# Performance work log

Measured on AMD Instinct MI355X. Metric: run time of the kernel, lower is better.

The kernel has to match this reference:

```python
import jax, jax.numpy as jnp
import numpy as np

NUM_HEADS = 4

def setup_inputs() -> dict:
    key = jax.random.key(0)
    ks = jax.random.split(key, 5)
    B, T, F, C = 2, 128, 256, 256
    # weights scaled ~1/sqrt(C) so softmax is not saturated
    s = 1.0 / np.sqrt(C)
    return {
        "x": jax.random.normal(ks[0], (B, T, F, C), jnp.float32),
        "w_in": jax.random.normal(ks[1], (3 * C, C), jnp.float32) * s,
        "b_in": jax.random.normal(ks[2], (3 * C,), jnp.float32) * 0.01,
        "w_out": jax.random.normal(ks[3], (C, C), jnp.float32) * s,
        "b_out": jax.random.normal(ks[4], (C,), jnp.float32) * 0.01,
        "band": 16,
    }

def reference(x, w_in, b_in, w_out, b_out, band):
    B, T, F, C = x.shape
    H = NUM_HEADS
    D = C // H
    x2 = x.reshape(B * T, F, C)  # attention over frequency, independent per (B,T)
    qkv = x2 @ w_in.T + b_in  # [BT, F, 3C]
    q, k, v = jnp.split(qkv, 3, axis=-1)
    def heads(t):
        return t.reshape(B * T, F, H, D).transpose(0, 2, 1, 3)  # [BT, H, F, D]
    q, k, v = heads(q), heads(k), heads(v)
    scores = jnp.einsum('bhid,bhjd->bhij', q, k) / jnp.sqrt(jnp.asarray(D, x.dtype))
    i = jnp.arange(F)[:, None]
    j = jnp.arange(F)[None, :]
    keep = jnp.abs(i - j) <= band  # banded locality mask [F, F]
    scores = jnp.where(keep, scores, -jnp.inf)
    attn = jax.nn.softmax(scores, axis=-1)
    out = jnp.einsum('bhij,bhjd->bhid', attn, v)  # [BT, H, F, D]
    out = out.transpose(0, 2, 1, 3).reshape(B * T, F, C)
    y = out @ w_out.T + b_out
    return y.reshape(B, T, F, C)
```

## Files before the change

### kernel.cpp

```cpp
#include <hip/hip_runtime.h>
#include <hip/hip_bf16.h>
#include <cstdint>

typedef unsigned int u32;
typedef __attribute__((ext_vector_type(8))) __bf16 bf16x8;
typedef __attribute__((ext_vector_type(4))) float f32x4;
typedef __attribute__((ext_vector_type(2))) _Float16 half2_t;
typedef __attribute__((ext_vector_type(4))) _Float16 half4;
typedef __attribute__((ext_vector_type(2))) __fp16 fp16x2;

#define BT_N 256
#define F_N 256
#define C_N 256
#define H_N 4
#define D_N 64
#define TC_N 768
#define M_N (BT_N * F_N)
#define VT_ST 268

__device__ __forceinline__ ushort f2bf(float f) {
  u32 u = __float_as_uint(f);
  u32 r = (u + 0x7fffu + ((u >> 16) & 1u)) >> 16;
  return (ushort)r;
}

__device__ __forceinline__ u32 pkbf(float a, float b) {
  return (u32)f2bf(a) | ((u32)f2bf(b) << 16);
}

__device__ __forceinline__ void gload_lds16(const ushort* g, ushort* l) {
  __builtin_amdgcn_global_load_lds(
      (const __attribute__((address_space(1))) u32*)g,
      (__attribute__((address_space(3))) u32*)l, 16, 0, 0);
}

#define WAITV(N) asm volatile("s_waitcnt vmcnt(" #N ")" ::: "memory")
#define BAR_IN  { __builtin_amdgcn_s_barrier(); \
                  asm volatile("" ::: "memory"); \
                  __builtin_amdgcn_sched_barrier(0); }
#define BAR_OUT { __builtin_amdgcn_sched_barrier(0); \
                  asm volatile("" ::: "memory"); \
                  __builtin_amdgcn_s_barrier(); }

__global__ __launch_bounds__(256) void cvt3_f32_bf16_k(
    const float* __restrict__ sx, ushort* __restrict__ dx, int nx4,
    const float* __restrict__ si, ushort* __restrict__ di, int ni4,
    const float* __restrict__ so, ushort* __restrict__ dq, int no4) {
  int idx = blockIdx.x * 256 + threadIdx.x;
  int stride = gridDim.x * 256;
  int ntot = nx4 + ni4 + no4;
  for (int i = idx; i < ntot; i += stride) {
    const float4* s;
    ushort* d;
    if (i < nx4) { s = (const float4*)sx + i; d = dx + (size_t)i * 4; }
    else if (i < nx4 + ni4) { int k = i - nx4; s = (const float4*)si + k; d = di + (size_t)k * 4; }
    else { int k = i - nx4 - ni4; s = (const float4*)so + k; d = dq + (size_t)k * 4; }
    float4 v = *s;
    *(uint2*)d = make_uint2(pkbf(v.x, v.y), pkbf(v.z, v.w));
  }
}

__global__ __launch_bounds__(256, 4) void gemm_qkv_sb(
    const ushort* __restrict__ Ap, const ushort* __restrict__ Bp,
    const float* __restrict__ bias, _Float16* __restrict__ Cp,
    int NTN, int nwg8) {
  __shared__ ushort smemH[128 * 64 * 2];

  const int tid = threadIdx.x;
  const int lane = tid & 63;
  const int wid = tid >> 6;
  const int wr = wid >> 1, wc = wid & 1;
  const int l15 = lane & 15, l4 = lane >> 4;
  const int b = blockIdx.x;
  const int bid = (b & 7) * nwg8 + (b >> 3);
  const int tm = bid / NTN;
  const int tn = bid - tm * NTN;
  const int rowBase = tm * 128, colBase = tn * 128;

  f32x4 acc[4][4] = {};

  const int ar = (tid >> 3);
  const int c8 = tid & 7;
  const int akk = ((c8 ^ (ar & 7)) << 3);
  const ushort* gB = Bp + (size_t)(colBase + ar) * 256 + akk;
  const ushort* gAh = Ap + (size_t)(rowBase + ar) * 256 + akk;

#pragma unroll
  for (int t = 0; t < 4; ++t) {
    const int k0 = t * 64;
#pragma unroll
    for (int c = 0; c < 4; ++c) {
      gload_lds16(gAh + (size_t)(c * 32) * 256 + k0,
                  smemH + (size_t)(c * 256 + (wid << 6)) * 8);
      gload_lds16(gB + (size_t)(c * 32) * 256 + k0,
                  smemH + 8192 + (size_t)(c * 256 + (wid << 6)) * 8);
    }
    __syncthreads();
    const ushort* As_ = smemH;
    const ushort* Bs_ = smemH + 8192;
#pragma unroll
    for (int kk = 0; kk < 2; ++kk) {
      bf16x8 af[4];
      bf16x8 bfr[4];
#pragma unroll
      for (int i2 = 0; i2 < 4; ++i2) {
        int row = wr * 64 + i2 * 16 + l15;
        af[i2] = *(const bf16x8*)(As_ + row * 64 + (((kk * 4 + l4) ^ (l15 & 7)) * 8));
      }
#pragma unroll
      for (int j2 = 0; j2 < 4; ++j2) {
        int row = wc * 64 + j2 * 16 + l15;
        bfr[j2] = *(const bf16x8*)(Bs_ + row * 64 + (((kk * 4 + l4) ^ (l15 & 7)) * 8));
      }
#pragma unroll
      for (int i2 = 0; i2 < 4; ++i2)
#pragma unroll
        for (int j2 = 0; j2 < 4; ++j2)
          acc[i2][j2] = __builtin_amdgcn_mfma_f32_16x16x32_bf16(
              af[i2], bfr[j2], acc[i2][j2], 0, 0, 0);
    }
    __syncthreads();
  }

  ushort* eb = smemH;
#pragma unroll
  for (int pass = 0; pass < 2; ++pass) {
#pragma unroll
    for (int jh = 0; jh < 2; ++jh) {
      const int i2 = pass * 2 + jh;
#pragma unroll
      for (int j2 = 0; j2 < 4; ++j2) {
        float bv = bias[colBase + wc * 64 + j2 * 16 + l15];
#pragma unroll
        for (int r = 0; r < 4; ++r) {
          _Float16 h = (_Float16)(acc[i2][j2][r] + bv);
          eb[(wr * 32 + jh * 16 + l4 * 4 + r) * 136 + wc * 64 + j2 * 16 + l15] =
              __builtin_bit_cast(ushort, h);
        }
      }
    }
    __syncthreads();
#pragma unroll
    for (int i = 0; i < 8; ++i) {
      int br = wid * 16 + 2 * i + (lane >> 5);
      int hl = lane & 31;
      uint2 d = *(const uint2*)(eb + br * 136 + hl * 4);
      int grow = rowBase + (br >> 5) * 64 + pass * 32 + (br & 31);
      *(uint2*)(Cp + (size_t)grow * TC_N + colBase + hl * 4) = d;
    }
    __syncthreads();
  }
}

template <typename OutT>
__global__ __launch_bounds__(256, 2) void gemm_bt(
    const ushort* __restrict__ Ap, const ushort* __restrict__ Bp,
    const float* __restrict__ bias, OutT* __restrict__ Cp,
    int N, int NTN, int nwg8) {
  constexpr bool F32OUT = (sizeof(OutT) == 4);
  constexpr int SMEM_BYTES = F32OUT ? 67584 : 65536;
  __shared__ char smem[SMEM_BYTES];
  ushort* smemH = (ushort*)smem;

  const int tid = threadIdx.x;
  const int lane = tid & 63;
  const int wid = tid >> 6;
  const int wr = wid >> 1, wc = wid & 1;
  const int l15 = lane & 15, l4 = lane >> 4;
  const int b = blockIdx.x;
  const int bid = (b & 7) * nwg8 + (b >> 3);
  const int tm = bid / NTN;
  const int tn = bid - tm * NTN;
  const int rowBase = tm * 128, colBase = tn * 128;

  f32x4 acc[4][4] = {};

  const int ar = (tid >> 3);
  const int c8 = tid & 7;
  const int akk = ((c8 ^ (ar & 7)) << 3);
  const ushort* gB = Bp + (size_t)(colBase + ar) * 256 + akk;
  const ushort* gAh = Ap + (size_t)(rowBase + ar) * 256 + akk;

#define STAGE_AB(buf, k0)                                                     \
  {                                                                           \
    ushort* As_ = smemH + (buf) * 8192;                                       \
    ushort* Bs_ = smemH + 16384 + (buf) * 8192;                               \
    _Pragma("unroll") for (int c = 0; c < 4; ++c) {                           \
      gload_lds16(gAh + (size_t)(c * 32) * 256 + (k0),                        \
                  As_ + (size_t)(c * 256 + (wid << 6)) * 8);                  \
      gload_lds16(gB + (size_t)(c * 32) * 256 + (k0),                         \
                  Bs_ + (size_t)(c * 256 + (wid << 6)) * 8);                  \
    }                                                                         \
  }

  STAGE_AB(0, 0);

  int cur = 0;
#pragma unroll
  for (int t = 0; t < 4; ++t) {
    if (t < 3) {
      STAGE_AB(cur ^ 1, (t + 1) * 64);
      WAITV(8);
    } else {
      WAITV(0);
    }
    BAR_IN;
    const ushort* As_ = smemH + cur * 8192;
    const ushort* Bs_ = smemH + 16384 + cur * 8192;
#pragma unroll
    for (int kk = 0; kk < 2; ++kk) {
      bf16x8 af[4];
      bf16x8 bfr[4];
#pragma unroll
      for (int i2 = 0; i2 < 4; ++i2) {
        int row = wr * 64 + i2 * 16 + l15;
        af[i2] = *(const bf16x8*)(As_ + row * 64 + (((kk * 4 + l4) ^ (l15 & 7)) * 8));
      }
#pragma unroll
      for (int j2 = 0; j2 < 4; ++j2) {
        int row = wc * 64 + j2 * 16 + l15;
        bfr[j2] = *(const bf16x8*)(Bs_ + row * 64 + (((kk * 4 + l4) ^ (l15 & 7)) * 8));
      }
#pragma unroll
      for (int i2 = 0; i2 < 4; ++i2)
#pragma unroll
        for (int j2 = 0; j2 < 4; ++j2)
          acc[i2][j2] = __builtin_amdgcn_mfma_f32_16x16x32_bf16(
              af[i2], bfr[j2], acc[i2][j2], 0, 0, 0);
    }
    BAR_OUT;
    cur ^= 1;
  }
#undef STAGE_AB

  __syncthreads();
  if constexpr (F32OUT) {
    float* eb = (float*)smem;
#pragma unroll
    for (int j2 = 0; j2 < 4; ++j2) {
      float bv = bias[colBase + wc * 64 + j2 * 16 + l15];
#pragma unroll
      for (int i2 = 0; i2 < 4; ++i2)
#pragma unroll
        for (int r = 0; r < 4; ++r)
          eb[(wr * 64 + i2 * 16 + l4 * 4 + r) * 132 + wc * 64 + j2 * 16 + l15] =
              acc[i2][j2][r] + bv;
    }
    __syncthreads();
#pragma unroll
    for (int i = 0; i < 32; ++i) {
      int row = wid * 32 + i;
      uint2 d = *(const uint2*)((const u32*)eb + row * 132 + lane * 2);
      *(uint2*)((float*)Cp + (size_t)(rowBase + row) * N + colBase + lane * 2) = d;
    }
  } else {
    ushort* eb = smemH;
#pragma unroll
    for (int j2 = 0; j2 < 4; ++j2) {
      float bv = bias[colBase + wc * 64 + j2 * 16 + l15];
#pragma unroll
      for (int i2 = 0; i2 < 4; ++i2)
#pragma unroll
        for (int r = 0; r < 4; ++r) {
          _Float16 h = (_Float16)(acc[i2][j2][r] + bv);
          eb[(wr * 64 + i2 * 16 + l4 * 4 + r) * 136 + wc * 64 + j2 * 16 + l15] =
              __builtin_bit_cast(ushort, h);
        }
    }
    __syncthreads();
#pragma unroll
    for (int i = 0; i < 16; ++i) {
      int row = wid * 32 + 2 * i + (lane >> 5);
      int hl = lane & 31;
      uint2 d = *(const uint2*)(eb + row * 136 + hl * 4);
      *(uint2*)((_Float16*)Cp + (size_t)(rowBase + row) * N + colBase + hl * 4) = d;
    }
  }
}

__global__ __launch_bounds__(256) void attn_mfma(
    const _Float16* __restrict__ qkv, ushort* __restrict__ aout) {
  __shared__ ushort smem[18432 + 64 * VT_ST];
  const int tid = threadIdx.x;
  const int bt = blockIdx.x >> 2;
  const int h = blockIdx.x & 3;
  const _Float16* base = qkv + (size_t)bt * 256 * 768 + h * 64;
  ushort* klds = smem;
  ushort* vlds = smem + 18432;

  {
    const int r0 = tid >> 3, c8 = tid & 7;
#pragma unroll
    for (int p = 0; p < 8; ++p) {
      int j = p * 32 + r0;
      const uint4 k4 = *(const uint4*)(base + (size_t)j * 768 + 256 + c8 * 8);
      *(uint4*)(klds + j * 72 + c8 * 8) = k4;
      const uint4 v4 = *(const uint4*)(base + (size_t)j * 768 + 512 + c8 * 8);
      const ushort* vh = (const ushort*)&v4;
      ushort* vtp = vlds + (c8 * 8) * VT_ST + j;
#pragma unroll
      for (int i = 0; i < 8; ++i) vtp[i * VT_ST] = vh[i];
    }
  }

  const int w = tid >> 6, lane = tid & 63;
  const int l15 = lane & 15, g = lane >> 4, g4 = g * 4;

  uint2 qf0[4], qf1[4], qf2[4], qf3[4];
  {
    const uint2* q0 = (const uint2*)(base + (size_t)(w * 64 + 0 * 16 + l15) * 768 + g4);
    const uint2* q1 = (const uint2*)(base + (size_t)(w * 64 + 1 * 16 + l15) * 768 + g4);
    const uint2* q2 = (const uint2*)(base + (size_t)(w * 64 + 2 * 16 + l15) * 768 + g4);
    const uint2* q3 = (const uint2*)(base + (size_t)(w * 64 + 3 * 16 + l15) * 768 + g4);
#pragma unroll
    for (int ks = 0; ks < 4; ++ks) {
      qf0[ks] = q0[ks * 4]; qf1[ks] = q1[ks * 4];
      qf2[ks] = q2[ks * 4]; qf3[ks] = q3[ks * 4];
    }
  }

  u32 bb = 0;
#pragma unroll
  for (int jt = 0; jt < 3; ++jt)
#pragma unroll
    for (int r = 0; r < 4; ++r) {
      int d = 16 * jt + g4 + r - 16 - l15;
      if (d >= -16 && d <= 16) bb |= 1u << (jt * 4 + r);
    }

  __syncthreads();

  const float SC = 0.18033688f;

#pragma unroll
  for (int rt = 0; rt < 4; ++rt) {
    const int R0 = w * 64 + rt * 16;
    const int Jc = R0 - 16;
    const uint2* qf = (rt == 0) ? qf0 : (rt == 1) ? qf1 : (rt == 2) ? qf2 : qf3;

    f32x4 st[3] = {};
#pragma unroll
    for (int jt = 0; jt < 3; ++jt) {
      int krow = Jc + 16 * jt + l15;
      krow = krow < 0 ? 0 : (krow > 255 ? 255 : krow);
      const ushort* kp = klds + krow * 72 + g4;
#pragma unroll
      for (int ks = 0; ks < 4; ++ks) {
        uint2 kf = *(const uint2*)(kp + ks * 16);
        st[jt] = __builtin_amdgcn_mfma_f32_16x16x16f16(
            __builtin_bit_cast(half4, kf), __builtin_bit_cast(half4, qf[ks]),
            st[jt], 0, 0, 0);
      }
    }

    float l_acc = 0.f;
    float pp[3][4];
#pragma unroll
    for (int jt = 0; jt < 3; ++jt)
#pragma unroll
      for (int r = 0; r < 4; ++r) {
        int jg = Jc + 16 * jt + g4 + r;
        bool keep = (((bb >> (jt * 4 + r)) & 1u) != 0) && (jg >= 0) && (jg < 256);
        float pv = keep ? __builtin_amdgcn_exp2f(st[jt][r] * SC) : 0.f;
        pp[jt][r] = pv;
        l_acc += pv;
      }
    l_acc += __shfl_xor(l_acc, 16, 64);
    l_acc += __shfl_xor(l_acc, 32, 64);
    const float inv = 1.f / l_acc;

    uint2 pf[3];
#pragma unroll
    for (int jt = 0; jt < 3; ++jt) {
      fp16x2 a = __builtin_amdgcn_cvt_pkrtz(pp[jt][0] * inv, pp[jt][1] * inv);
      fp16x2 c = __builtin_amdgcn_cvt_pkrtz(pp[jt][2] * inv, pp[jt][3] * inv);
      pf[jt].x = __builtin_bit_cast(u32, a);
      pf[jt].y = __builtin_bit_cast(u32, c);
    }

    f32x4 ot[4] = {};
#pragma unroll
    for (int kt = 0; kt < 3; ++kt) {
      int jb = Jc + 16 * kt + g4;
      jb = jb < 0 ? 0 : (jb > 252 ? 252 : jb);
#pragma unroll
      for (int mt = 0; mt < 4; ++mt) {
        uint2 vfr = *(const uint2*)(vlds + (16 * mt + l15) * VT_ST + jb);
        ot[mt] = __builtin_amdgcn_mfma_f32_16x16x16f16(
            __builtin_bit_cast(half4, vfr), __builtin_bit_cast(half4, pf[kt]),
            ot[mt], 0, 0, 0);
      }
    }

    ushort* orow = aout + (size_t)(bt * 256 + R0 + l15) * 256 + h * 64 + g4;
#pragma unroll
    for (int mt = 0; mt < 4; ++mt) {
      u32 lo = (u32)f2bf(ot[mt][0]) | ((u32)f2bf(ot[mt][1]) << 16);
      u32 hi = (u32)f2bf(ot[mt][2]) | ((u32)f2bf(ot[mt][3]) << 16);
      *(uint2*)(orow + mt * 16) = make_uint2(lo, hi);
    }
  }
}

extern "C" void kernel_launch(void* const* d_in, const int* in_sizes, int n_in,
                              void* d_out, int out_size, void* d_ws, size_t ws_size,
                              hipStream_t stream) {
  const float* x = (const float*)d_in[0];
  const float* w_in = (const float*)d_in[1];
  const float* b_in = (const float*)d_in[2];
  const float* w_out = (const float*)d_in[3];
  const float* b_out = (const float*)d_in[4];
  float* y = (float*)d_out;

  char* ws = (char*)d_ws;
  const size_t qkv_bytes = (size_t)M_N * TC_N * 2;
  const size_t xb_bytes = (size_t)M_N * C_N * 2;
  _Float16* qkv = (_Float16*)ws;
  ushort* xb = (ushort*)(ws + qkv_bytes);
  ushort* attn = xb;
  ushort* winb = (ushort*)(ws + qkv_bytes + xb_bytes);
  ushort* woutb = winb + TC_N * C_N;

  cvt3_f32_bf16_k<<<2048, 256, 0, stream>>>(x, xb, M_N * C_N / 4,
                                            w_in, winb, TC_N * C_N / 4,
                                            w_out, woutb, C_N * C_N / 4);

  gemm_qkv_sb<<<(M_N / 128) * (TC_N / 128), 256, 0, stream>>>(
      xb, winb, b_in, qkv, TC_N / 128, (M_N / 128) * (TC_N / 128) / 8);

  attn_mfma<<<BT_N * H_N, 256, 0, stream>>>(qkv, attn);

  gemm_bt<float><<<(M_N / 128) * (C_N / 128), 256, 0, stream>>>(
      attn, woutb, b_out, y, C_N, C_N / 128, (M_N / 128) * (C_N / 128) / 8);
}
```

Measured before the change: 99.81 us.

## Single-buffer output GEMM for higher occupancy and pack V transpose writes

Replaces the templated double-buffered output GEMM with a single-buffered variant that uses about 33KB of LDS. It also writes its fp32 epilogue in two half passes and raises launch bounds from 2 to 4 blocks per CU, trading load/compute overlap for more resident waves. The attention kernel's V transpose into LDS now loads two adjacent rows and writes packed 32-bit words instead of scattered 16-bit stores, cutting LDS store count.

```diff
diff --git a/kernel.cpp b/kernel.cpp
--- a/kernel.cpp
+++ b/kernel.cpp
@@ -5,7 +5,6 @@
 typedef unsigned int u32;
 typedef __attribute__((ext_vector_type(8))) __bf16 bf16x8;
 typedef __attribute__((ext_vector_type(4))) float f32x4;
-typedef __attribute__((ext_vector_type(2))) _Float16 half2_t;
 typedef __attribute__((ext_vector_type(4))) _Float16 half4;
 typedef __attribute__((ext_vector_type(2))) __fp16 fp16x2;
 
@@ -33,14 +32,6 @@
       (const __attribute__((address_space(1))) u32*)g,
       (__attribute__((address_space(3))) u32*)l, 16, 0, 0);
 }
-
-#define WAITV(N) asm volatile("s_waitcnt vmcnt(" #N ")" ::: "memory")
-#define BAR_IN  { __builtin_amdgcn_s_barrier(); \
-                  asm volatile("" ::: "memory"); \
-                  __builtin_amdgcn_sched_barrier(0); }
-#define BAR_OUT { __builtin_amdgcn_sched_barrier(0); \
-                  asm volatile("" ::: "memory"); \
-                  __builtin_amdgcn_s_barrier(); }
 
 __global__ __launch_bounds__(256) void cvt3_f32_bf16_k(
     const float* __restrict__ sx, ushort* __restrict__ dx, int nx4,
@@ -152,14 +143,11 @@
   }
 }
 
-template <typename OutT>
-__global__ __launch_bounds__(256, 2) void gemm_bt(
+__global__ __launch_bounds__(256, 4) void gemm_out_sb(
     const ushort* __restrict__ Ap, const ushort* __restrict__ Bp,
-    const float* __restrict__ bias, OutT* __restrict__ Cp,
-    int N, int NTN, int nwg8) {
-  constexpr bool F32OUT = (sizeof(OutT) == 4);
-  constexpr int SMEM_BYTES = F32OUT ? 67584 : 65536;
-  __shared__ char smem[SMEM_BYTES];
+    const float* __restrict__ bias, float* __restrict__ Cp,
+    int NTN, int nwg8) {
+  __shared__ char smem[64 * 132 * 4];
   ushort* smemH = (ushort*)smem;
 
   const int tid = threadIdx.x;
@@ -181,32 +169,19 @@
   const ushort* gB = Bp + (size_t)(colBase + ar) * 256 + akk;
   const ushort* gAh = Ap + (size_t)(rowBase + ar) * 256 + akk;
 
-#define STAGE_AB(buf, k0)                                                     \
-  {                                                                           \
-    ushort* As_ = smemH + (buf) * 8192;                                       \
-    ushort* Bs_ = smemH + 16384 + (buf) * 8192;                               \
-    _Pragma("unroll") for (int c = 0; c < 4; ++c) {                           \
-      gload_lds16(gAh + (size_t)(c * 32) * 256 + (k0),                        \
-                  As_ + (size_t)(c * 256 + (wid << 6)) * 8);                  \
-      gload_lds16(gB + (size_t)(c * 32) * 256 + (k0),                         \
-                  Bs_ + (size_t)(c * 256 + (wid << 6)) * 8);                  \
-    }                                                                         \
-  }
-
-  STAGE_AB(0, 0);
-
-  int cur = 0;
 #pragma unroll
   for (int t = 0; t < 4; ++t) {
-    if (t < 3) {
-      STAGE_AB(cur ^ 1, (t + 1) * 64);
-      WAITV(8);
-    } else {
-      WAITV(0);
-    }
-    BAR_IN;
-    const ushort* As_ = smemH + cur * 8192;
-    const ushort* Bs_ = smemH + 16384 + cur * 8192;
+    const int k0 = t * 64;
+#pragma unroll
+    for (int c = 0; c < 4; ++c) {
+      gload_lds16(gAh + (size_t)(c * 32) * 256 + k0,
+                  smemH + (size_t)(c * 256 + (wid << 6)) * 8);
+      gload_lds16(gB + (size_t)(c * 32) * 256 + k0,
+                  smemH + 8192 + (size_t)(c * 256 + (wid << 6)) * 8);
+    }
+    __syncthreads();
+    const ushort* As_ = smemH;
+    const ushort* Bs_ = smemH + 8192;
 #pragma unroll
     for (int kk = 0; kk < 2; ++kk) {
       bf16x8 af[4];
@@ -228,53 +203,33 @@
           acc[i2][j2] = __builtin_amdgcn_mfma_f32_16x16x32_bf16(
               af[i2], bfr[j2], acc[i2][j2], 0, 0, 0);
     }
-    BAR_OUT;
-    cur ^= 1;
-  }
-#undef STAGE_AB
-
-  __syncthreads();
-  if constexpr (F32OUT) {
-    float* eb = (float*)smem;
-#pragma unroll
-    for (int j2 = 0; j2 < 4; ++j2) {
-      float bv = bias[colBase + wc * 64 + j2 * 16 + l15];
-#pragma unroll
-      for (int i2 = 0; i2 < 4; ++i2)
+    __syncthreads();
+  }
+
+  float* eb = (float*)smem;
+#pragma unroll
+  for (int pass = 0; pass < 2; ++pass) {
+#pragma unroll
+    for (int jh = 0; jh < 2; ++jh) {
+      const int i2 = pass * 2 + jh;
+#pragma unroll
+      for (int j2 = 0; j2 < 4; ++j2) {
+        float bv = bias[colBase + wc * 64 + j2 * 16 + l15];
 #pragma unroll
         for (int r = 0; r < 4; ++r)
-          eb[(wr * 64 + i2 * 16 + l4 * 4 + r) * 132 + wc * 64 + j2 * 16 + l15] =
+          eb[(wr * 32 + jh * 16 + l4 * 4 + r) * 132 + wc * 64 + j2 * 16 + l15] =
               acc[i2][j2][r] + bv;
-    }
-    __syncthreads();
-#pragma unroll
-    for (int i = 0; i < 32; ++i) {
-      int row = wid * 32 + i;
-      uint2 d = *(const uint2*)((const u32*)eb + row * 132 + lane * 2);
-      *(uint2*)((float*)Cp + (size_t)(rowBase + row) * N + colBase + lane * 2) = d;
-    }
-  } else {
-    ushort* eb = smemH;
-#pragma unroll
-    for (int j2 = 0; j2 < 4; ++j2) {
-      float bv = bias[colBase + wc * 64 + j2 * 16 + l15];
-#pragma unroll
-      for (int i2 = 0; i2 < 4; ++i2)
-#pragma unroll
-        for (int r = 0; r < 4; ++r) {
-          _Float16 h = (_Float16)(acc[i2][j2][r] + bv);
-          eb[(wr * 64 + i2 * 16 + l4 * 4 + r) * 136 + wc * 64 + j2 * 16 + l15] =
-              __builtin_bit_cast(ushort, h);
-        }
+      }
     }
     __syncthreads();
 #pragma unroll
     for (int i = 0; i < 16; ++i) {
-      int row = wid * 32 + 2 * i + (lane >> 5);
-      int hl = lane & 31;
-      uint2 d = *(const uint2*)(eb + row * 136 + hl * 4);
-      *(uint2*)((_Float16*)Cp + (size_t)(rowBase + row) * N + colBase + hl * 4) = d;
-    }
+      int br = wid * 16 + i;
+      uint2 d = *(const uint2*)((const u32*)eb + br * 132 + lane * 2);
+      int grow = rowBase + (br >> 5) * 64 + pass * 32 + (br & 31);
+      *(uint2*)(Cp + (size_t)grow * C_N + colBase + lane * 2) = d;
+    }
+    __syncthreads();
   }
 }
 
@@ -290,16 +245,24 @@
 
   {
     const int r0 = tid >> 3, c8 = tid & 7;
+    const int pr2 = tid >> 4, dq = tid & 15;
 #pragma unroll
     for (int p = 0; p < 8; ++p) {
       int j = p * 32 + r0;
       const uint4 k4 = *(const uint4*)(base + (size_t)j * 768 + 256 + c8 * 8);
       *(uint4*)(klds + j * 72 + c8 * 8) = k4;
-      const uint4 v4 = *(const uint4*)(base + (size_t)j * 768 + 512 + c8 * 8);
-      const ushort* vh = (const ushort*)&v4;
-      ushort* vtp = vlds + (c8 * 8) * VT_ST + j;
-#pragma unroll
-      for (int i = 0; i < 8; ++i) vtp[i * VT_ST] = vh[i];
+      int j0 = p * 32 + pr2 * 2;
+      uint2 va = *(const uint2*)(base + (size_t)j0 * 768 + 512 + dq * 4);
+      uint2 vb = *(const uint2*)(base + (size_t)(j0 + 1) * 768 + 512 + dq * 4);
+      u32 w0 = (va.x & 0xffffu) | (vb.x << 16);
+      u32 w1 = (va.x >> 16) | (vb.x & 0xffff0000u);
+      u32 w2 = (va.y & 0xffffu) | (vb.y << 16);
+      u32 w3 = (va.y >> 16) | (vb.y & 0xffff0000u);
+      int d0 = dq * 4;
+      *(u32*)(vlds + (d0 + 0) * VT_ST + j0) = w0;
+      *(u32*)(vlds + (d0 + 1) * VT_ST + j0) = w1;
+      *(u32*)(vlds + (d0 + 2) * VT_ST + j0) = w2;
+      *(u32*)(vlds + (d0 + 3) * VT_ST + j0) = w3;
     }
   }
 
@@ -430,6 +393,6 @@
 
   attn_mfma<<<BT_N * H_N, 256, 0, stream>>>(qkv, attn);
 
-  gemm_bt<float><<<(M_N / 128) * (C_N / 128), 256, 0, stream>>>(
-      attn, woutb, b_out, y, C_N, C_N / 128, (M_N / 128) * (C_N / 128) / 8);
-}
+  gemm_out_sb<<<(M_N / 128) * (C_N / 128), 256, 0, stream>>>(
+      attn, woutb, b_out, y, C_N / 128, (M_N / 128) * (C_N / 128) / 8);
+}
```

New measurement: 99.28 us. About the same (-0.5%).
